# Performance work log

Measured on AMD Instinct MI355X. Metric: run time of the kernel, lower is better.

Reference implementation:

```python
import jax, jax.numpy as jnp
import numpy as np

B, L, C, H = 8, 2048, 256, 4
D = C // H  # head_dim = 64
EPS = 1e-5


def setup_inputs() -> dict:
    key = jax.random.key(0)
    ks = jax.random.split(key, 16)
    s = lambda fan_in: 1.0 / np.sqrt(fan_in)
    inp = {
        'x0': jax.random.normal(ks[0], (B, L, C), jnp.float32),
        'x1': jax.random.normal(ks[1], (B, L, C), jnp.float32),
        # attention projections (stored as (in, out); torch Linear is x @ W.T + b)
        'Wqk': jax.random.normal(ks[2], (C, C), jnp.float32) * s(C),
        'bqk': jax.random.normal(ks[3], (C,), jnp.float32) * s(C),
        'Wv': jax.random.normal(ks[4], (C, C), jnp.float32) * s(C),
        'bv': jax.random.normal(ks[5], (C,), jnp.float32) * s(C),
        'Wout': jax.random.normal(ks[6], (C, C), jnp.float32) * s(C),
        'bout': jax.random.normal(ks[7], (C,), jnp.float32) * s(C),
        # shared FFN: Linear(2C->2C) -> LayerNorm -> GELU -> Linear(2C->C)
        'W1': jax.random.normal(ks[8], (2 * C, 2 * C), jnp.float32) * s(2 * C),
        'b1': jax.random.normal(ks[9], (2 * C,), jnp.float32) * s(2 * C),
        'ln_g': jnp.ones((2 * C,), jnp.float32),
        'ln_b': jnp.zeros((2 * C,), jnp.float32),
        'W2': jax.random.normal(ks[10], (2 * C, C), jnp.float32) * s(2 * C),
        'b2': jax.random.normal(ks[11], (C,), jnp.float32) * s(2 * C),
    }
    return inp


def _heads(t):
    # (B, L, C) -> (B, H, L, D)
    b, l, _ = t.shape
    return t.reshape(b, l, H, D).transpose(0, 2, 1, 3)


def _merge(t):
    # (B, H, L, D) -> (B, L, C)
    b, h, l, d = t.shape
    return t.transpose(0, 2, 1, 3).reshape(b, l, h * d)


def _ffn(z, W1, b1, ln_g, ln_b, W2, b2):
    h = z @ W1 + b1
    mu = jnp.mean(h, axis=-1, keepdims=True)
    var = jnp.var(h, axis=-1, keepdims=True)
    h = (h - mu) * jax.lax.rsqrt(var + EPS) * ln_g + ln_b
    h = jax.nn.gelu(h, approximate=False)
    return h @ W2 + b2


def reference(x0, x1, Wqk, bqk, Wv, bv, Wout, bout, W1, b1, ln_g, ln_b, W2, b2):
    scale_sqrt = D ** (-0.25)  # sqrt(head_dim**-0.5), applied to both sides
    qk0 = _heads(x0 @ Wqk + bqk) * scale_sqrt  # (B,H,M,D)
    qk1 = _heads(x1 @ Wqk + bqk) * scale_sqrt  # (B,H,N,D)
    v0 = _heads(x0 @ Wv + bv)
    v1 = _heads(x1 @ Wv + bv)

    # single shared similarity matrix (LightGlue trick)
    sim = jnp.einsum('bhid,bhjd->bhij', qk0, qk1)  # (B,H,M,N)
    attn01 = jax.nn.softmax(sim, axis=-1)           # rows: A->B
    attn10 = jax.nn.softmax(sim, axis=-2)           # cols: B->A (softmax of sim^T along last dim)
    m0 = jnp.einsum('bhij,bhjd->bhid', attn01, v1)  # (B,H,M,D)
    m1 = jnp.einsum('bhij,bhid->bhjd', attn10, v0)  # (B,H,N,D)

    m0 = _merge(m0) @ Wout + bout
    m1 = _merge(m1) @ Wout + bout

    x0_out = x0 + _ffn(jnp.concatenate([x0, m0], axis=-1), W1, b1, ln_g, ln_b, W2, b2)
    x1_out = x1 + _ffn(jnp.concatenate([x1, m1], axis=-1), W1, b1, ln_g, ln_b, W2, b2)
    return (x0_out, x1_out)
```

## Files before the change

kernel.cpp:

```cpp
#include <hip/hip_runtime.h>
#include <hip/hip_bf16.h>

typedef _Float16 f16;
typedef _Float16 f16x8 __attribute__((ext_vector_type(8)));
typedef _Float16 f16x4 __attribute__((ext_vector_type(4)));
typedef _Float16 f16x2 __attribute__((ext_vector_type(2)));
typedef float f32x4 __attribute__((ext_vector_type(4)));
typedef float f32x2 __attribute__((ext_vector_type(2)));

#define MFMA16(a, b, c) __builtin_amdgcn_mfma_f32_16x16x32_f16((a), (b), (c), 0, 0, 0)

__device__ __forceinline__ void load16(const void* g, void* l) {
    __builtin_amdgcn_global_load_lds((const __attribute__((address_space(1))) void*)g,
                                     (__attribute__((address_space(3))) void*)l, 16, 0, 0);
}

__device__ __forceinline__ unsigned int pkrtz(float a, float b) {
    return __builtin_bit_cast(unsigned int, __builtin_amdgcn_cvt_pkrtz(a, b));
}

__global__ __launch_bounds__(256) void k_prep(const float* __restrict__ x0,
                                              const float* __restrict__ x1,
                                              const float* __restrict__ Wqk,
                                              const float* __restrict__ Wv,
                                              const float* __restrict__ W1,
                                              const float* __restrict__ W2,
                                              const float* __restrict__ Wout,
                                              const float* __restrict__ b1,
                                              const float* __restrict__ bout,
                                              f16* __restrict__ xh, f16* __restrict__ wcat_t,
                                              f16* __restrict__ w1t, f16* __restrict__ w1bt,
                                              f16* __restrict__ w2t, f16* __restrict__ woutf16,
                                              float* __restrict__ bias_eff) {
    __shared__ float red[4];
    const int blk = blockIdx.x, tid = threadIdx.x;
    if (blk < 8192) {
        size_t i = ((size_t)blk * 256 + tid) * 4;
        const float* src = (i < 4194304) ? (x0 + i) : (x1 + (i - 4194304));
        float4 v = *(const float4*)src;
        f16x4 o = {(f16)v.x, (f16)v.y, (f16)v.z, (f16)v.w};
        *(f16x4*)(xh + i) = o;
    } else if (blk < 8704) {
        int n = blk - 8192;
        const float* W = (n < 256) ? Wqk : Wv;
        wcat_t[n * 256 + tid] = (f16)W[tid * 256 + (n & 255)];
    } else if (blk < 9216) {
        int n = blk - 8704;
        w1t[n * 512 + tid] = (f16)W1[tid * 512 + n];
    } else if (blk < 9728) {
        int n = blk - 9216;
        w1bt[n * 256 + tid] = (f16)W1[(256 + tid) * 512 + n];
    } else if (blk < 10240) {
        int j = blk - 9728;
        int n = j >> 1, k = (j & 1) * 256 + tid;
        w2t[n * 512 + k] = (f16)W2[k * 256 + n];
    } else if (blk < 10496) {
        int o = (blk - 10240) * 256 + tid;
        woutf16[o] = (f16)Wout[o];
    } else {
        int n = blk - 10496;
        float s = bout[tid] * W1[(size_t)(256 + tid) * 512 + n];
#pragma unroll
        for (int off = 1; off < 64; off <<= 1) s += __shfl_xor(s, off);
        int wave = tid >> 6, lane = tid & 63;
        if (lane == 0) red[wave] = s;
        __syncthreads();
        if (tid == 0) bias_eff[n] = b1[n] + red[0] + red[1] + red[2] + red[3];
    }
}

__global__ __launch_bounds__(256, 2) void k_gemm(const f16* __restrict__ A1,
                                                 const f16* __restrict__ A2, int ksplit,
                                                 int strideA, const f16* __restrict__ Bt, int K,
                                                 int N, const float* __restrict__ bias1,
                                                 const float* __restrict__ bias2, int mode,
                                                 void* __restrict__ out1, void* __restrict__ out2,
                                                 const f16* __restrict__ resh) {
    const int bm0 = blockIdx.x * 128;
    const int bn0 = blockIdx.y * 256;
    __shared__ f16 As[2][4096];
    __shared__ f16 Bs[2][8192];
    const int tid = threadIdx.x;
    const int lane = tid & 63, wave = tid >> 6;
    const int quad = lane >> 4, l16 = lane & 15;
    const int wm0 = (wave & 1) * 64, wn0 = (wave >> 1) * 128;
    const int axor = l16 & 3;

    f32x4 acc[4][8];
#pragma unroll
    for (int tm = 0; tm < 4; tm++)
#pragma unroll
        for (int tn = 0; tn < 8; tn++) acc[tm][tn] = (f32x4){0.f, 0.f, 0.f, 0.f};

    auto stage = [&](int buf, int kt) {
        const int k0 = kt * 32;
        const f16* Ab = (k0 < ksplit) ? A1 : A2;
        const int koff = (k0 < ksplit) ? k0 : k0 - ksplit;
#pragma unroll
        for (int rd = 0; rd < 2; rd++) {
            const int cbase = rd * 256 + wave * 64;
            const int c = cbase + lane;
            const int row = c >> 2, col = (c & 3) ^ (row & 3);
            load16(Ab + (size_t)(bm0 + row) * strideA + koff + col * 8, &As[buf][cbase * 8]);
        }
#pragma unroll
        for (int rd = 0; rd < 4; rd++) {
            const int cbase = rd * 256 + wave * 64;
            const int c = cbase + lane;
            const int row = c >> 2, col = (c & 3) ^ (row & 3);
            load16(Bt + (size_t)(bn0 + row) * K + k0 + col * 8, &Bs[buf][cbase * 8]);
        }
    };

    const int NT = K >> 5;
    stage(0, 0);
    __syncthreads();
    for (int kt = 0; kt < NT; kt++) {
        const int cur = kt & 1;
        if (kt + 1 < NT) stage(cur ^ 1, kt + 1);
        f16x8 af[4], bf[8];
#pragma unroll
        for (int t = 0; t < 4; t++)
            af[t] = *(const f16x8*)&As[cur][(wm0 + t * 16 + l16) * 32 + (quad ^ axor) * 8];
#pragma unroll
        for (int t = 0; t < 8; t++)
            bf[t] = *(const f16x8*)&Bs[cur][(wn0 + t * 16 + l16) * 32 + (quad ^ axor) * 8];
#pragma unroll
        for (int tm = 0; tm < 4; tm++)
#pragma unroll
            for (int tn = 0; tn < 8; tn++) acc[tm][tn] = MFMA16(bf[tn], af[tm], acc[tm][tn]);
        __syncthreads();
    }

#pragma unroll
    for (int tm = 0; tm < 4; tm++) {
        const int m = bm0 + wm0 + tm * 16 + l16;
#pragma unroll
        for (int tn = 0; tn < 8; tn++) {
            const int n = bn0 + wn0 + tn * 16 + quad * 4;
            f32x4 v = acc[tm][tn];
            if (mode == 0) {
                const int s = m >> 14, r14 = m & 16383, b = r14 >> 11, l = r14 & 2047;
                if (n < 256) {
                    float4 bi = *(const float4*)(bias1 + n);
                    const int h = n >> 6, d = n & 63;
                    const size_t hh = (size_t)((s * 8 + b) * 4 + h);
                    f16x4 o = {(f16)((v[0] + bi.x) * 0.42466090f),
                               (f16)((v[1] + bi.y) * 0.42466090f),
                               (f16)((v[2] + bi.z) * 0.42466090f),
                               (f16)((v[3] + bi.w) * 0.42466090f)};
                    *(f16x4*)((f16*)out1 + (hh * 2048 + l) * 64 + d) = o;
                } else {
                    const int n2 = n - 256;
                    float4 bi = *(const float4*)(bias2 + n2);
                    const int h = n2 >> 6, d = n2 & 63;
                    const size_t hh = (size_t)((s * 8 + b) * 4 + h);
                    f16* o2 = (f16*)out2 + (hh * 64 + d) * 2048 + l;
                    o2[0] = (f16)(v[0] + bi.x);
                    o2[2048] = (f16)(v[1] + bi.y);
                    o2[4096] = (f16)(v[2] + bi.z);
                    o2[6144] = (f16)(v[3] + bi.w);
                }
            } else if (mode == 2) {
                float4 bi = *(const float4*)(bias1 + n);
                f16x4 o = {(f16)(v[0] + bi.x), (f16)(v[1] + bi.y), (f16)(v[2] + bi.z),
                           (f16)(v[3] + bi.w)};
                *(f16x4*)((f16*)out1 + (size_t)m * N + n) = o;
            } else if (mode == 3) {
                float4 bi = *(const float4*)(bias1 + n);
                f16x4 rr = *(const f16x4*)(resh + (size_t)m * 256 + n);
                float4 o = {v[0] + bi.x + (float)rr[0], v[1] + bi.y + (float)rr[1],
                            v[2] + bi.z + (float)rr[2], v[3] + bi.w + (float)rr[3]};
                *(float4*)((float*)out1 + (size_t)m * 256 + n) = o;
            } else {
                f16x4 o = {(f16)v[0], (f16)v[1], (f16)v[2], (f16)v[3]};
                *(f16x4*)((f16*)out1 + (size_t)m * 512 + 256 + n) = o;
            }
        }
    }
}

__global__ __launch_bounds__(256, 4) void k_flash(const f16* __restrict__ qkbuf,
                                                  const f16* __restrict__ vtbuf,
                                                  f16* __restrict__ mbuf) {
    const int z = blockIdx.z;
    const int bh = blockIdx.x;
    const int qt = blockIdx.y;
    const size_t HSZ = 2048 * 64;
    const size_t SSZ = 32 * HSZ;
    const f16* Q = qkbuf + (z ? SSZ : 0) + bh * HSZ;
    const f16* Kp = qkbuf + (z ? 0 : SSZ) + bh * HSZ;
    const f16* Vt = vtbuf + (z ? 0 : SSZ) + bh * HSZ;
    f16* Mo = mbuf + (size_t)z * (16384 * 256);

    __shared__ f16 Ks[2][4096];
    __shared__ f16 Vs[2][4096];

    const int tid = threadIdx.x, lane = tid & 63, wave = tid >> 6;
    const int quad = lane >> 4, l16 = lane & 15;
    const int srow = lane >> 3;
    const int slc = (lane & 7) ^ (srow & 7);
    const int sw = l16 & 7;

    const int q0 = qt * 128 + wave * 32;
    f16x8 qf[2][2];
#pragma unroll
    for (int tq = 0; tq < 2; tq++)
#pragma unroll
        for (int kk = 0; kk < 2; kk++)
            qf[tq][kk] =
                *(const f16x8*)(Q + (size_t)(q0 + tq * 16 + l16) * 64 + kk * 32 + quad * 8);

    const f16* kb[2] = {&Ks[0][l16 * 64 + ((0 + quad) ^ sw) * 8],
                        &Ks[0][l16 * 64 + ((4 + quad) ^ sw) * 8]};
    const f16* vb[2] = {&Vs[0][l16 * 64 + ((0 + quad) ^ sw) * 8],
                        &Vs[0][l16 * 64 + ((4 + quad) ^ sw) * 8]};

    const f16* pK0 = Kp + (size_t)(wave * 16 + srow) * 64 + slc * 8;
    const f16* pK1 = pK0 + 8 * 64;
    const f16* pV0 = Vt + (size_t)(wave * 16 + srow) * 2048 + slc * 8;
    const f16* pV1 = pV0 + 8 * 2048;
    f16* kd0 = &Ks[0][(wave * 2 + 0) * 512];
    f16* kd1 = &Ks[0][(wave * 2 + 1) * 512];
    f16* vd0 = &Vs[0][(wave * 2 + 0) * 512];
    f16* vd1 = &Vs[0][(wave * 2 + 1) * 512];

    auto stage = [&](int buf, int kv0) {
        load16(pK0 + (size_t)kv0 * 64, kd0 + buf * 4096);
        load16(pK1 + (size_t)kv0 * 64, kd1 + buf * 4096);
        load16(pV0 + kv0, vd0 + buf * 4096);
        load16(pV1 + kv0, vd1 + buf * 4096);
    };

    f32x4 oacc[4][2];
#pragma unroll
    for (int td = 0; td < 4; td++)
#pragma unroll
        for (int tq = 0; tq < 2; tq++) oacc[td][tq] = (f32x4){0.f, 0.f, 0.f, 0.f};
    f32x4 oext[2] = {{0.f, 0.f, 0.f, 0.f}, {0.f, 0.f, 0.f, 0.f}};
    const f16x8 vones = {(f16)1.f, (f16)1.f, (f16)1.f, (f16)1.f,
                         (f16)1.f, (f16)1.f, (f16)1.f, (f16)1.f};

    stage(0, 0);
    __syncthreads();

    auto body = [&](int cur, int t) {
        if (t < 31) stage(cur ^ 1, (t + 1) * 64);

        f32x4 sacc[4][2];
#pragma unroll
        for (int tkv = 0; tkv < 4; tkv++)
#pragma unroll
            for (int tq = 0; tq < 2; tq++)
                sacc[tkv][tq] = (f32x4){-8.f, -8.f, -8.f, -8.f};
#pragma unroll
        for (int kk = 0; kk < 2; kk++) {
#pragma unroll
            for (int tkv = 0; tkv < 4; tkv++) {
                f16x8 ka = *(const f16x8*)(kb[kk] + cur * 4096 + tkv * 1024);
#pragma unroll
                for (int tq = 0; tq < 2; tq++)
                    sacc[tkv][tq] = MFMA16(ka, qf[tq][kk], sacc[tkv][tq]);
            }
        }

        f16x8 bfrag[2][2];
#pragma unroll
        for (int blk = 0; blk < 2; blk++) {
#pragma unroll
            for (int tq = 0; tq < 2; tq++) {
                unsigned int rg[2][2];
#pragma unroll
                for (int tt = 0; tt < 2; tt++) {
                    const int tkv = blk * 2 + tt;
                    float p0 = __builtin_amdgcn_exp2f(sacc[tkv][tq][0]);
                    float p1 = __builtin_amdgcn_exp2f(sacc[tkv][tq][1]);
                    float p2 = __builtin_amdgcn_exp2f(sacc[tkv][tq][2]);
                    float p3 = __builtin_amdgcn_exp2f(sacc[tkv][tq][3]);
                    rg[tt][0] = pkrtz(p0, p1);
                    rg[tt][1] = pkrtz(p2, p3);
                }
                auto ab0 = __builtin_amdgcn_permlane32_swap(rg[0][0], rg[1][0], false, false);
                auto uw0 = __builtin_amdgcn_permlane16_swap(ab0[0], ab0[1], false, false);
                auto ab1 = __builtin_amdgcn_permlane32_swap(rg[0][1], rg[1][1], false, false);
                auto uw1 = __builtin_amdgcn_permlane16_swap(ab1[0], ab1[1], false, false);
                union {
                    unsigned int u[4];
                    f16x8 v;
                } bb;
                bb.u[0] = uw0[0];
                bb.u[1] = uw1[0];
                bb.u[2] = uw0[1];
                bb.u[3] = uw1[1];
                bfrag[blk][tq] = bb.v;
            }
        }

#pragma unroll
        for (int blk = 0; blk < 2; blk++) {
#pragma unroll
            for (int td = 0; td < 4; td++) {
                f16x8 va = *(const f16x8*)(vb[blk] + cur * 4096 + td * 1024);
#pragma unroll
                for (int tq = 0; tq < 2; tq++)
                    oacc[td][tq] = MFMA16(va, bfrag[blk][tq], oacc[td][tq]);
            }
#pragma unroll
            for (int tq = 0; tq < 2; tq++)
                oext[tq] = MFMA16(vones, bfrag[blk][tq], oext[tq]);
        }
        __syncthreads();
    };

    for (int t = 0; t < 32; t += 2) {
        body(0, t);
        body(1, t + 1);
    }

    const int b = bh >> 2, h = bh & 3;
#pragma unroll
    for (int tq = 0; tq < 2; tq++) {
        const float inv = 1.f / oext[tq][0];
        const int q = q0 + tq * 16 + l16;
        const size_t base = ((size_t)(b * 2048 + q)) * 256 + h * 64;
#pragma unroll
        for (int td = 0; td < 4; td++) {
            f16x4 o = {(f16)(oacc[td][tq][0] * inv), (f16)(oacc[td][tq][1] * inv),
                       (f16)(oacc[td][tq][2] * inv), (f16)(oacc[td][tq][3] * inv)};
            *(f16x4*)(Mo + base + td * 16 + quad * 4) = o;
        }
    }
}

__global__ __launch_bounds__(256) void k_ln_gelu(f16* __restrict__ h,
                                                 const float* __restrict__ g,
                                                 const float* __restrict__ bb) {
    const int tid = threadIdx.x, wave = tid >> 6, lane = tid & 63;
    const size_t row = (size_t)blockIdx.x * 4 + wave;
    f16* hr = h + row * 512 + lane * 8;
    f16x8 v = *(const f16x8*)hr;
    float x[8];
    float s = 0.f, sq = 0.f;
#pragma unroll
    for (int i = 0; i < 8; i++) {
        x[i] = (float)v[i];
        s += x[i];
        sq += x[i] * x[i];
    }
#pragma unroll
    for (int off = 1; off < 64; off <<= 1) {
        s += __shfl_xor(s, off);
        sq += __shfl_xor(sq, off);
    }
    const float mu = s * (1.f / 512.f);
    const float var = sq * (1.f / 512.f) - mu * mu;
    const float rstd = rsqrtf(var + 1e-5f);
    float4 g0 = *(const float4*)(g + lane * 8), g1 = *(const float4*)(g + lane * 8 + 4);
    float4 b0 = *(const float4*)(bb + lane * 8), b1 = *(const float4*)(bb + lane * 8 + 4);
    float gg[8] = {g0.x, g0.y, g0.z, g0.w, g1.x, g1.y, g1.z, g1.w};
    float bv[8] = {b0.x, b0.y, b0.z, b0.w, b1.x, b1.y, b1.z, b1.w};
#pragma unroll
    for (int i = 0; i < 8; i++) {
        float a = (x[i] - mu) * rstd * gg[i] + bv[i];
        a = 0.5f * a * (1.f + erff(a * 0.70710678118f));
        v[i] = (f16)a;
    }
    *(f16x8*)hr = v;
}


extern "C" void kernel_launch(void* const* d_in, const int* in_sizes, int n_in, void* d_out,
                              int out_size, void* d_ws, size_t ws_size, hipStream_t stream) {
    const float* x0 = (const float*)d_in[0];
    const float* x1 = (const float*)d_in[1];
    const float* Wqk = (const float*)d_in[2];
    const float* bqk = (const float*)d_in[3];
    const float* Wv = (const float*)d_in[4];
    const float* bv = (const float*)d_in[5];
    const float* Wout = (const float*)d_in[6];
    const float* bout = (const float*)d_in[7];
    const float* W1 = (const float*)d_in[8];
    const float* b1 = (const float*)d_in[9];
    const float* lng = (const float*)d_in[10];
    const float* lnb = (const float*)d_in[11];
    const float* W2 = (const float*)d_in[12];
    const float* b2 = (const float*)d_in[13];
    float* out = (float*)d_out;

    char* ws = (char*)d_ws;
    f16* xh = (f16*)(ws);
    f16* qk = (f16*)(ws + 16777216);
    f16* vt = (f16*)(ws + 33554432);
    f16* mbuf = (f16*)(ws + 50331648);
    f16* hbuf = qk;
    f16* w1bt = (f16*)(ws + 16777216);
    f16* woutf16 = w1bt + 131072;
    f16* wcat_t = (f16*)(ws + 67108864);
    f16* w1t = wcat_t + 131072;
    f16* w2t = w1t + 262144;
    float* bias_eff = (float*)(w2t + 131072);

    k_prep<<<11008, 256, 0, stream>>>(x0, x1, Wqk, Wv, W1, W2, Wout, b1, bout, xh, wcat_t, w1t,
                                      w1bt, w2t, woutf16, bias_eff);
    k_gemm<<<dim3(4, 1), 256, 0, stream>>>(w1bt, w1bt, 1 << 30, 256, woutf16, 256, 256, nullptr,
                                           nullptr, 4, w1t, nullptr, nullptr);
    k_gemm<<<dim3(256, 2), 256, 0, stream>>>(xh, xh, 1 << 30, 256, wcat_t, 256, 512, bqk, bv, 0,
                                             qk, vt, nullptr);
    k_flash<<<dim3(32, 16, 2), 256, 0, stream>>>(qk, vt, mbuf);
    k_gemm<<<dim3(256, 2), 256, 0, stream>>>(xh, mbuf, 256, 256, w1t, 512, 512, bias_eff,
                                             nullptr, 2, hbuf, nullptr, nullptr);
    k_ln_gelu<<<8192, 256, 0, stream>>>(hbuf, lng, lnb);
    k_gemm<<<dim3(256, 1), 256, 0, stream>>>(hbuf, hbuf, 1 << 30, 512, w2t, 512, 256, b2,
                                             nullptr, 3, out, nullptr, xh);
}
```

Before: 307.1 us.

## Fold weight-fusion GEMM into QKV GEMM launch and relax flash-attention waits

The small Wout·W1 fusion GEMM now runs as extra blocks appended to the QKV projection launch, which removes one kernel launch and its serialization gap. Its workspace buffer moves to a region that no earlier kernel in the sequence still uses. In the flash kernel, __syncthreads is replaced by raw s_barrier with an explicit vmcnt(4) wait, so the next tile's prefetch can stay in flight while the current tile is computed. The risk is ordering: correctness now depends on the manual waitcnt counting the global-to-LDS loads exactly.

```diff
diff --git a/kernel.cpp b/kernel.cpp
--- a/kernel.cpp
+++ b/kernel.cpp
@@ -75,9 +75,30 @@
                                                  int N, const float* __restrict__ bias1,
                                                  const float* __restrict__ bias2, int mode,
                                                  void* __restrict__ out1, void* __restrict__ out2,
-                                                 const f16* __restrict__ resh) {
-    const int bm0 = blockIdx.x * 128;
-    const int bn0 = blockIdx.y * 256;
+                                                 const f16* __restrict__ resh,
+                                                 const f16* __restrict__ pgA,
+                                                 const f16* __restrict__ pgBt,
+                                                 f16* __restrict__ pgOut) {
+    int bm0 = blockIdx.x * 128;
+    int bn0 = blockIdx.y * 256;
+    if (pgOut != nullptr && blockIdx.x >= 256) {
+        if (blockIdx.y != 0) return;
+        A1 = pgA;
+        A2 = pgA;
+        ksplit = 1 << 30;
+        strideA = 256;
+        Bt = pgBt;
+        K = 256;
+        N = 256;
+        bias1 = nullptr;
+        bias2 = nullptr;
+        mode = 4;
+        out1 = pgOut;
+        out2 = nullptr;
+        resh = nullptr;
+        bm0 = (blockIdx.x - 256) * 128;
+        bn0 = 0;
+    }
     __shared__ f16 As[2][4096];
     __shared__ f16 Bs[2][8192];
     const int tid = threadIdx.x;
@@ -242,10 +263,15 @@
                          (f16)1.f, (f16)1.f, (f16)1.f, (f16)1.f};
 
     stage(0, 0);
-    __syncthreads();
 
     auto body = [&](int cur, int t) {
-        if (t < 31) stage(cur ^ 1, (t + 1) * 64);
+        if (t < 31) {
+            stage(cur ^ 1, (t + 1) * 64);
+            asm volatile("s_waitcnt vmcnt(4)" ::: "memory");
+        } else {
+            asm volatile("s_waitcnt vmcnt(0)" ::: "memory");
+        }
+        __builtin_amdgcn_s_barrier();
 
         f32x4 sacc[4][2];
 #pragma unroll
@@ -309,7 +335,7 @@
             for (int tq = 0; tq < 2; tq++)
                 oext[tq] = MFMA16(vones, bfrag[blk][tq], oext[tq]);
         }
-        __syncthreads();
+        __builtin_amdgcn_s_barrier();
     };
 
     for (int t = 0; t < 32; t += 2) {
@@ -393,7 +419,7 @@
     f16* vt = (f16*)(ws + 33554432);
     f16* mbuf = (f16*)(ws + 50331648);
     f16* hbuf = qk;
-    f16* w1bt = (f16*)(ws + 16777216);
+    f16* w1bt = (f16*)(ws + 50331648);
     f16* woutf16 = w1bt + 131072;
     f16* wcat_t = (f16*)(ws + 67108864);
     f16* w1t = wcat_t + 131072;
@@ -402,14 +428,14 @@
 
     k_prep<<<11008, 256, 0, stream>>>(x0, x1, Wqk, Wv, W1, W2, Wout, b1, bout, xh, wcat_t, w1t,
                                       w1bt, w2t, woutf16, bias_eff);
-    k_gemm<<<dim3(4, 1), 256, 0, stream>>>(w1bt, w1bt, 1 << 30, 256, woutf16, 256, 256, nullptr,
-                                           nullptr, 4, w1t, nullptr, nullptr);
-    k_gemm<<<dim3(256, 2), 256, 0, stream>>>(xh, xh, 1 << 30, 256, wcat_t, 256, 512, bqk, bv, 0,
-                                             qk, vt, nullptr);
+    k_gemm<<<dim3(260, 2), 256, 0, stream>>>(xh, xh, 1 << 30, 256, wcat_t, 256, 512, bqk, bv, 0,
+                                             qk, vt, nullptr, w1bt, woutf16, w1t);
     k_flash<<<dim3(32, 16, 2), 256, 0, stream>>>(qk, vt, mbuf);
     k_gemm<<<dim3(256, 2), 256, 0, stream>>>(xh, mbuf, 256, 256, w1t, 512, 512, bias_eff,
-                                             nullptr, 2, hbuf, nullptr, nullptr);
+                                             nullptr, 2, hbuf, nullptr, nullptr, nullptr,
+                                             nullptr, nullptr);
     k_ln_gelu<<<8192, 256, 0, stream>>>(hbuf, lng, lnb);
     k_gemm<<<dim3(256, 1), 256, 0, stream>>>(hbuf, hbuf, 1 << 30, 512, w2t, 512, 256, b2,
-                                             nullptr, 3, out, nullptr, xh);
-}
+                                             nullptr, 3, out, nullptr, xh, nullptr, nullptr,
+                                             nullptr);
+}
```

Measured after the change: 305.4 us. About the same (-0.6%).
